# Kernel tuning notes

Hardware: AMD Instinct MI355X
Metric: run time of the kernel (lower is better)

Reference implementation:

```python
import jax, jax.numpy as jnp
from jax import lax
import numpy as np

D_MODEL = 1024
D_INNER = 2048   # expand=2
D_STATE = 16
D_CONV = 4
DT_RANK = 64     # ceil(1024/16)
N_LAYERS = 24
PATCH = 16
H0 = W0 = 24     # 384 // 16
BATCH = 2
IMG = 384


def setup_inputs() -> dict:
    key = jax.random.key(0)
    ks = jax.random.split(key, 12)
    def rn(k, shape, scale=0.02):
        return jax.random.normal(k, shape, jnp.float32) * scale
    A_init = jnp.broadcast_to(jnp.arange(1, D_STATE + 1, dtype=jnp.float32),
                              (N_LAYERS, D_INNER, D_STATE))
    return {
        "x": jax.random.normal(ks[0], (BATCH, 3, IMG, IMG), jnp.float32),
        "patch_w": rn(ks[1], (D_MODEL, 3, PATCH, PATCH)),
        "patch_b": jnp.zeros((D_MODEL,), jnp.float32),
        "cls_token": rn(ks[2], (1, 1, D_MODEL)),
        "pos_embed": rn(ks[3], (1, 1 + H0 * W0, D_MODEL)),
        "ln_w": jnp.ones((N_LAYERS, D_MODEL), jnp.float32),
        "ln_b": jnp.zeros((N_LAYERS, D_MODEL), jnp.float32),
        "in_proj_w": rn(ks[4], (N_LAYERS, 2 * D_INNER, D_MODEL)),
        "conv_w": rn(ks[5], (N_LAYERS, D_INNER, D_CONV), 0.1),
        "conv_b": jnp.zeros((N_LAYERS, D_INNER), jnp.float32),
        "x_proj_w": rn(ks[6], (N_LAYERS, DT_RANK + 2 * D_STATE, D_INNER)),
        "dt_proj_w": rn(ks[7], (N_LAYERS, D_INNER, DT_RANK), 0.1),
        "dt_proj_b": rn(ks[8], (N_LAYERS, D_INNER), 0.5),
        "A_log": jnp.log(A_init),
        "D_skip": jnp.ones((N_LAYERS, D_INNER), jnp.float32),
        "out_proj_w": rn(ks[9], (N_LAYERS, D_MODEL, D_INNER)),
    }


def _layernorm(x, w, b):
    m = x.mean(-1, keepdims=True)
    xc = x - m
    v = (xc * xc).mean(-1, keepdims=True)
    return xc * lax.rsqrt(v + 1e-5) * w + b


def _mamba_block(tok, p):
    # tok: [B, L, D]
    lw, lb, ipw, cw, cb, xpw, dpw, dpb, alog, dsk, opw = p
    h = _layernorm(tok, lw, lb)
    xz = jnp.einsum('bld,ed->ble', h, ipw)          # [B, L, 2*d_inner]
    xc, z = jnp.split(xz, 2, axis=-1)
    # causal depthwise conv1d over sequence, kernel D_CONV
    u = lax.conv_general_dilated(
        xc.transpose(0, 2, 1), cw[:, None, :], (1,), [(D_CONV - 1, 0)],
        dimension_numbers=('NCH', 'OIH', 'NCH'), feature_group_count=D_INNER)
    u = jax.nn.silu(u + cb[None, :, None]).transpose(0, 2, 1)  # [B, L, d_inner]
    dbl = jnp.einsum('ble,fe->blf', u, xpw)         # [B, L, dt_rank + 2*d_state]
    dt = jax.nn.softplus(jnp.einsum('blr,dr->bld', dbl[..., :DT_RANK], dpw) + dpb)
    Bm = dbl[..., DT_RANK:DT_RANK + D_STATE]        # [B, L, d_state]
    Cm = dbl[..., DT_RANK + D_STATE:]               # [B, L, d_state]
    A = -jnp.exp(alog)                              # [d_inner, d_state]

    def step(hst, inp):
        dt_t, B_t, C_t, u_t = inp                   # [B,d_inner],[B,ds],[B,ds],[B,d_inner]
        hst = jnp.exp(dt_t[..., None] * A) * hst + (dt_t * u_t)[..., None] * B_t[:, None, :]
        y_t = jnp.einsum('bds,bs->bd', hst, C_t)
        return hst, y_t

    h0 = jnp.zeros((tok.shape[0], D_INNER, D_STATE), tok.dtype)
    _, ys = lax.scan(step, h0, (dt.transpose(1, 0, 2), Bm.transpose(1, 0, 2),
                                Cm.transpose(1, 0, 2), u.transpose(1, 0, 2)))
    y = ys.transpose(1, 0, 2) + dsk * u
    y = y * jax.nn.silu(z)
    return tok + jnp.einsum('ble,de->bld', y, opw)


def reference(x, patch_w, patch_b, cls_token, pos_embed, ln_w, ln_b, in_proj_w,
              conv_w, conv_b, x_proj_w, dt_proj_w, dt_proj_b, A_log, D_skip,
              out_proj_w):
    # patch embed: conv stride=kernel=16
    feat = lax.conv_general_dilated(x, patch_w, (PATCH, PATCH), 'VALID',
                                    dimension_numbers=('NCHW', 'OIHW', 'NCHW'))
    feat = feat + patch_b[None, :, None, None]
    B, Dm, H, W = feat.shape
    tokens = feat.reshape(B, Dm, H * W).transpose(0, 2, 1)
    tokens = jnp.concatenate([jnp.broadcast_to(cls_token, (B, 1, Dm)), tokens], 1)
    # bilinear (half-pixel, align_corners=False) pos-embed interpolation
    pp = pos_embed[:, 1:, :].reshape(1, H0, W0, Dm)
    pp = jax.image.resize(pp, (1, H, W, Dm), method='bilinear').reshape(1, H * W, Dm)
    tokens = tokens + jnp.concatenate([pos_embed[:, :1, :], pp], 1)
    params = (ln_w, ln_b, in_proj_w, conv_w, conv_b, x_proj_w, dt_proj_w,
              dt_proj_b, A_log, D_skip, out_proj_w)
    blk = jax.checkpoint(_mamba_block)
    tokens, _ = lax.scan(lambda t, p: (blk(t, p), None), tokens, params)
    return tokens
```

## Files before the change

### kernel.cpp

```cpp
#include <hip/hip_runtime.h>
#include <hip/hip_bf16.h>
#include <math.h>

#define BATCH 2
#define LSEQ 577
#define DM 1024
#define DI 2048
#define DSTATE 16
#define DTR 64
#define NLAYERS 24
#define NP 576
#define MROWS 1154
#define NC 32
#define LC 19

typedef __attribute__((ext_vector_type(8))) short short8v;
typedef __attribute__((ext_vector_type(4))) float f32x4;

__device__ __forceinline__ ushort f2bf(float f) {
  unsigned int b = __float_as_uint(f);
  return (ushort)((b + 0x7FFFu + ((b >> 16) & 1u)) >> 16);
}
__device__ __forceinline__ float bf2f(ushort u) {
  return __uint_as_float(((unsigned int)u) << 16);
}
__device__ __forceinline__ void gload16(const void* g, void* l) {
  __builtin_amdgcn_global_load_lds(
      (const __attribute__((address_space(1))) unsigned int*)g,
      (__attribute__((address_space(3))) unsigned int*)l, 16, 0, 0);
}
__device__ __forceinline__ void cvt16(const float* g, char* ldsrow, int bb, int bswz) {
  float4 v0 = *(const float4*)(g);
  float4 v1 = *(const float4*)(g + 4);
  float4 v2 = *(const float4*)(g + 8);
  float4 v3 = *(const float4*)(g + 12);
  short8v c0 = {(short)f2bf(v0.x), (short)f2bf(v0.y), (short)f2bf(v0.z), (short)f2bf(v0.w),
                (short)f2bf(v1.x), (short)f2bf(v1.y), (short)f2bf(v1.z), (short)f2bf(v1.w)};
  short8v c1 = {(short)f2bf(v2.x), (short)f2bf(v2.y), (short)f2bf(v2.z), (short)f2bf(v2.w),
                (short)f2bf(v3.x), (short)f2bf(v3.y), (short)f2bf(v3.z), (short)f2bf(v3.w)};
  *(short8v*)(ldsrow + (bb ^ bswz)) = c0;
  *(short8v*)(ldsrow + ((bb + 16) ^ bswz)) = c1;
}

__global__ void f2bf_k(const float* __restrict__ in, ushort* __restrict__ out, int n) {
  for (int i = (blockIdx.x * 256 + threadIdx.x) * 4; i < n; i += gridDim.x * 1024) {
    float4 v = *(const float4*)(in + i);
    ushort4 o;
    o.x = f2bf(v.x); o.y = f2bf(v.y); o.z = f2bf(v.z); o.w = f2bf(v.w);
    *(ushort4*)(out + i) = o;
  }
}

template<int AF32, int MODE>
__global__ __launch_bounds__(256) void gemm64(
    const void* __restrict__ Ap_, int lda,
    const ushort* __restrict__ Bw, int ldb,
    float* __restrict__ C, int ldc,
    int M, int N, int K,
    const float* __restrict__ bias, const float* __restrict__ pos,
    ushort* __restrict__ o16a, ushort* __restrict__ o16b)
{
  __shared__ char lds[AF32 ? 24576 : 49152];
  int tid = threadIdx.x;
  int lane = tid & 63, w = tid >> 6;
  int bm = blockIdx.y * 64, bn = blockIdx.x * 128;

  int srow = tid >> 3;
  int scol = ((tid & 7) ^ (srow & 7)) << 3;

  const ushort* gb0 = Bw + (size_t)(bn + srow) * ldb + scol;
  const ushort* gb1 = Bw + (size_t)(bn + 32 + srow) * ldb + scol;
  const ushort* gb2 = Bw + (size_t)(bn + 64 + srow) * ldb + scol;
  const ushort* gb3 = Bw + (size_t)(bn + 96 + srow) * ldb + scol;

  const ushort* ga0 = nullptr; const ushort* ga1 = nullptr;
  const float* gAf = nullptr; char* ldsArow = nullptr; int bb = 0, bswz = 0;
  if (!AF32) {
    const ushort* Abf = (const ushort*)Ap_;
    int ra0 = bm + srow;      if (ra0 > M - 1) ra0 = M - 1;
    int ra1 = bm + 32 + srow; if (ra1 > M - 1) ra1 = M - 1;
    ga0 = Abf + (size_t)ra0 * lda + scol;
    ga1 = Abf + (size_t)ra1 * lda + scol;
  } else {
    int brow = tid >> 2;
    int be0 = (tid & 3) << 4;
    bb = be0 << 1; bswz = (brow & 7) << 4;
    int raf = bm + brow; if (raf > M - 1) raf = M - 1;
    gAf = (const float*)Ap_ + (size_t)raf * lda + be0;
    ldsArow = lds + brow * 128;
  }

  int wr = w >> 1, wc = w & 1;
  int fr = lane & 15;
  int fsw = (fr & 7) << 4;
  int fk = (lane >> 4) << 4;

  f32x4 acc[2][4];
  #pragma unroll
  for (int m = 0; m < 2; ++m)
    #pragma unroll
    for (int n = 0; n < 4; ++n) acc[m][n] = (f32x4){0.f, 0.f, 0.f, 0.f};

  if constexpr (!AF32) {
    auto stage = [&](int buf, int k0) {
      char* p = lds + buf * 24576;
      gload16(ga0 + k0, p + (w << 10));
      gload16(ga1 + k0, p + 4096 + (w << 10));
      gload16(gb0 + k0, p + 8192 + (w << 10));
      gload16(gb1 + k0, p + 12288 + (w << 10));
      gload16(gb2 + k0, p + 16384 + (w << 10));
      gload16(gb3 + k0, p + 20480 + (w << 10));
    };
    int nk = K >> 6;
    stage(0, 0);
    for (int k = 0; k < nk; ++k) {
      int cur = k & 1;
      if (k + 1 < nk) {
        stage(cur ^ 1, (k + 1) << 6);
        asm volatile("s_waitcnt vmcnt(6)" ::: "memory");
      } else {
        asm volatile("s_waitcnt vmcnt(0)" ::: "memory");
      }
      __builtin_amdgcn_s_barrier();
      char* p = lds + cur * 24576;
      #pragma unroll
      for (int ks = 0; ks < 2; ++ks) {
        int cb = (ks * 64 + fk) ^ fsw;
        short8v af[2], bf[4];
        #pragma unroll
        for (int m = 0; m < 2; ++m)
          af[m] = *(const short8v*)(p + (wr * 32 + m * 16 + fr) * 128 + cb);
        #pragma unroll
        for (int n = 0; n < 4; ++n)
          bf[n] = *(const short8v*)(p + 8192 + (wc * 64 + n * 16 + fr) * 128 + cb);
        #pragma unroll
        for (int m = 0; m < 2; ++m)
          #pragma unroll
          for (int n = 0; n < 4; ++n)
            acc[m][n] = __builtin_amdgcn_mfma_f32_16x16x32_bf16(af[m], bf[n], acc[m][n], 0, 0, 0);
      }
      __builtin_amdgcn_s_barrier();
    }
  } else {
    for (int k0 = 0; k0 < K; k0 += 64) {
      cvt16(gAf + k0, ldsArow, bb, bswz);
      gload16(gb0 + k0, lds + 8192 + (w << 10));
      gload16(gb1 + k0, lds + 12288 + (w << 10));
      gload16(gb2 + k0, lds + 16384 + (w << 10));
      gload16(gb3 + k0, lds + 20480 + (w << 10));
      __syncthreads();
      #pragma unroll
      for (int ks = 0; ks < 2; ++ks) {
        int cb = (ks * 64 + fk) ^ fsw;
        short8v af[2], bf[4];
        #pragma unroll
        for (int m = 0; m < 2; ++m)
          af[m] = *(const short8v*)(lds + (wr * 32 + m * 16 + fr) * 128 + cb);
        #pragma unroll
        for (int n = 0; n < 4; ++n)
          bf[n] = *(const short8v*)(lds + 8192 + (wc * 64 + n * 16 + fr) * 128 + cb);
        #pragma unroll
        for (int m = 0; m < 2; ++m)
          #pragma unroll
          for (int n = 0; n < 4; ++n)
            acc[m][n] = __builtin_amdgcn_mfma_f32_16x16x32_bf16(af[m], bf[n], acc[m][n], 0, 0, 0);
      }
      __syncthreads();
    }
  }

  #pragma unroll
  for (int m = 0; m < 2; ++m) {
    int rb = bm + wr * 32 + m * 16 + ((lane >> 4) << 2);
    #pragma unroll
    for (int j = 0; j < 4; ++j) {
      int r = rb + j;
      if (r >= M) break;
      #pragma unroll
      for (int n2 = 0; n2 < 4; ++n2) {
        int n = bn + wc * 64 + n2 * 16 + fr;
        float v = acc[m][n2][j];
        if (MODE == 1) {
          C[(size_t)r * ldc + n] += v;
        } else if (MODE == 3) {
          int b = r / NP, p = r % NP;
          C[((size_t)(b * LSEQ + 1 + p)) * ldc + n] = v + bias[n] + pos[(size_t)(1 + p) * ldc + n];
        } else if (MODE == 4) {
          if (n < DI) o16a[(size_t)r * DI + n] = f2bf(v);
          else        o16b[(size_t)r * DI + n - DI] = f2bf(v);
        } else {
          float t = v + bias[n];
          o16a[(size_t)r * N + n] = f2bf((t > 20.f) ? t : log1pf(__expf(t)));
        }
      }
    }
  }
}

__global__ __launch_bounds__(256) void xproj_k(
    const ushort* __restrict__ A, const ushort* __restrict__ W,
    float* __restrict__ C, int M)
{
  __shared__ char lds[20480];
  int tid = threadIdx.x;
  int lane = tid & 63, w = tid >> 6;
  int bm = blockIdx.y * 64;
  int kbase = blockIdx.x * 256;

  int srow = tid >> 3;
  int scol = ((tid & 7) ^ (srow & 7)) << 3;
  int ra0 = bm + srow;      if (ra0 > M - 1) ra0 = M - 1;
  int ra1 = bm + 32 + srow; if (ra1 > M - 1) ra1 = M - 1;
  const ushort* ga0 = A + (size_t)ra0 * DI + kbase + scol;
  const ushort* ga1 = A + (size_t)ra1 * DI + kbase + scol;
  char* la0 = lds + (w << 10);
  char* la1 = lds + 4096 + (w << 10);
  const ushort* gb0 = W + (size_t)(srow)      * DI + kbase + scol;
  const ushort* gb1 = W + (size_t)(srow + 32) * DI + kbase + scol;
  const ushort* gb2 = W + (size_t)(srow + 64) * DI + kbase + scol;
  char* lb0 = lds + 8192 + (w << 10);
  char* lb1 = lds + 12288 + (w << 10);
  char* lb2 = lds + 16384 + (w << 10);

  int fr = lane & 15;
  int fsw = (fr & 7) << 4;
  int fk = (lane >> 4) << 4;
  int arow = (w * 16 + fr) * 128;

  f32x4 acc[6];
  #pragma unroll
  for (int n = 0; n < 6; ++n) acc[n] = (f32x4){0.f, 0.f, 0.f, 0.f};

  for (int k0 = 0; k0 < 256; k0 += 64) {
    gload16(ga0 + k0, la0);
    gload16(ga1 + k0, la1);
    gload16(gb0 + k0, lb0);
    gload16(gb1 + k0, lb1);
    gload16(gb2 + k0, lb2);
    __syncthreads();
    #pragma unroll
    for (int ks = 0; ks < 2; ++ks) {
      int cb = (ks * 64 + fk) ^ fsw;
      short8v af = *(const short8v*)(lds + arow + cb);
      #pragma unroll
      for (int n = 0; n < 6; ++n) {
        short8v bf = *(const short8v*)(lds + 8192 + (n * 16 + fr) * 128 + cb);
        acc[n] = __builtin_amdgcn_mfma_f32_16x16x32_bf16(af, bf, acc[n], 0, 0, 0);
      }
    }
    __syncthreads();
  }

  int rb = bm + w * 16 + ((lane >> 4) << 2);
  #pragma unroll
  for (int j = 0; j < 4; ++j) {
    int r = rb + j;
    if (r >= M) break;
    #pragma unroll
    for (int n = 0; n < 6; ++n)
      atomicAdd(C + (size_t)r * 96 + n * 16 + fr, acc[n][j]);
  }
}

__global__ void im2col_k(const float* __restrict__ x, ushort* __restrict__ patches) {
  int idx = blockIdx.x * 256 + threadIdx.x;
  if (idx >= BATCH * NP * 768) return;
  int col = idx % 768, row = idx / 768;
  int b = row / NP, p = row % NP;
  int ph = p / 24, pw = p % 24;
  int c = col >> 8, r = col & 255, kh = r >> 4, kw = r & 15;
  patches[idx] = f2bf(x[(((size_t)(b * 3 + c) * 384) + ph * 16 + kh) * 384 + pw * 16 + kw]);
}

__global__ void cls_k(const float* __restrict__ cls, const float* __restrict__ pos,
                      float* __restrict__ out) {
  int n = blockIdx.x * 256 + threadIdx.x;
  if (n >= DM) return;
  float v = cls[n] + pos[n];
  out[n] = v;
  out[(size_t)LSEQ * DM + n] = v;
}

__global__ __launch_bounds__(256) void ln_k(const float* __restrict__ tok,
    const float* __restrict__ w, const float* __restrict__ bsh,
    ushort* __restrict__ h) {
  int row = blockIdx.x;
  const float* xr = tok + (size_t)row * DM;
  int tid = threadIdx.x;
  float v[4];
  #pragma unroll
  for (int i = 0; i < 4; ++i) v[i] = xr[tid + 256 * i];
  float s = v[0] + v[1] + v[2] + v[3];
  float s2 = v[0] * v[0] + v[1] * v[1] + v[2] * v[2] + v[3] * v[3];
  #pragma unroll
  for (int off = 32; off; off >>= 1) { s += __shfl_xor(s, off); s2 += __shfl_xor(s2, off); }
  __shared__ float ps[4], ps2[4];
  if ((tid & 63) == 0) { ps[tid >> 6] = s; ps2[tid >> 6] = s2; }
  __syncthreads();
  s = ps[0] + ps[1] + ps[2] + ps[3];
  s2 = ps2[0] + ps2[1] + ps2[2] + ps2[3];
  float mean = s * (1.f / DM);
  float var = s2 * (1.f / DM) - mean * mean;
  float inv = rsqrtf(var + 1e-5f);
  #pragma unroll
  for (int i = 0; i < 4; ++i) {
    int c = tid + 256 * i;
    h[(size_t)row * DM + c] = f2bf((v[i] - mean) * inv * w[c] + bsh[c]);
  }
}

__global__ void conv_silu_k(const ushort* __restrict__ xc, const float* __restrict__ cw,
                            const float* __restrict__ cb, ushort* __restrict__ ubf,
                            float* __restrict__ dbl0) {
  int idx = blockIdx.x * 256 + threadIdx.x;
  if (idx < MROWS * 96) dbl0[idx] = 0.f;
  if (idx >= MROWS * DI) return;
  int d = idx & (DI - 1);
  int ro = idx >> 11;
  int l = ro % LSEQ;
  float acc = cb[d];
  #pragma unroll
  for (int k = 0; k < 4; ++k) {
    int ll = l - 3 + k;
    if (ll >= 0) acc += bf2f(xc[(size_t)(ro - 3 + k) * DI + d]) * cw[d * 4 + k];
  }
  ubf[idx] = f2bf(acc / (1.f + __expf(-acc)));
}

__global__ __launch_bounds__(256) void scan1_k(
    const ushort* __restrict__ dt, const ushort* __restrict__ ubf,
    const float* __restrict__ dbl, const float* __restrict__ alog,
    ushort* __restrict__ Ap, ushort* __restrict__ He)
{
  int d = blockIdx.x * 256 + threadIdx.x;
  int b = blockIdx.y, c = blockIdx.z;
  int t0 = c * LC, t1 = t0 + LC; if (t1 > LSEQ) t1 = LSEQ;
  float Ad[DSTATE], ap[DSTATE], h[DSTATE];
  #pragma unroll
  for (int s = 0; s < DSTATE; ++s) {
    Ad[s] = -__expf(alog[d * DSTATE + s]); ap[s] = 1.f; h[s] = 0.f;
  }
  for (int t = t0; t < t1; ++t) {
    size_t ro = (size_t)b * LSEQ + t;
    float dtv = bf2f(dt[ro * DI + d]);
    float du = dtv * bf2f(ubf[ro * DI + d]);
    const float* r = dbl + ro * 96;
    #pragma unroll
    for (int s = 0; s < DSTATE; ++s) {
      float e = __expf(dtv * Ad[s]);
      h[s] = e * h[s] + du * r[64 + s];
      ap[s] *= e;
    }
  }
  size_t o = (((size_t)(b * NC + c)) * DI + d) * DSTATE;
  #pragma unroll
  for (int s = 0; s < DSTATE; ++s) { Ap[o + s] = f2bf(ap[s]); He[o + s] = f2bf(h[s]); }
}

__global__ __launch_bounds__(256) void scan2_k(
    ushort* __restrict__ Ap, const ushort* __restrict__ He)
{
  int ds = blockIdx.x * 256 + threadIdx.x;
  int b = blockIdx.y;
  float h = 0.f;
  #pragma unroll
  for (int g = 0; g < NC; g += 8) {
    float apg[8], heg[8];
    #pragma unroll
    for (int j = 0; j < 8; ++j) {
      size_t oo = ((size_t)(b * NC + g + j)) * DI * DSTATE + ds;
      apg[j] = bf2f(Ap[oo]); heg[j] = bf2f(He[oo]);
    }
    #pragma unroll
    for (int j = 0; j < 8; ++j) {
      size_t oo = ((size_t)(b * NC + g + j)) * DI * DSTATE + ds;
      Ap[oo] = f2bf(h);
      h = apg[j] * h + heg[j];
    }
  }
}

__global__ __launch_bounds__(256) void scan3_k(
    const ushort* __restrict__ dt, const ushort* __restrict__ ubf,
    const float* __restrict__ dbl, const ushort* __restrict__ zbf,
    const float* __restrict__ alog, const float* __restrict__ dsk,
    const ushort* __restrict__ H0, ushort* __restrict__ y)
{
  int d = blockIdx.x * 256 + threadIdx.x;
  int b = blockIdx.y, c = blockIdx.z;
  int t0 = c * LC, t1 = t0 + LC; if (t1 > LSEQ) t1 = LSEQ;
  float Ad[DSTATE], h[DSTATE];
  size_t o = (((size_t)(b * NC + c)) * DI + d) * DSTATE;
  #pragma unroll
  for (int s = 0; s < DSTATE; ++s) {
    Ad[s] = -__expf(alog[d * DSTATE + s]);
    h[s] = bf2f(H0[o + s]);
  }
  float Dv = dsk[d];
  for (int t = t0; t < t1; ++t) {
    size_t ro = (size_t)b * LSEQ + t;
    float dtv = bf2f(dt[ro * DI + d]);
    float uv = bf2f(ubf[ro * DI + d]);
    float du = dtv * uv;
    const float* r = dbl + ro * 96;
    float yv = 0.f;
    #pragma unroll
    for (int s = 0; s < DSTATE; ++s) {
      h[s] = __expf(dtv * Ad[s]) * h[s] + du * r[64 + s];
      yv += h[s] * r[80 + s];
    }
    float z = bf2f(zbf[ro * DI + d]);
    y[ro * DI + d] = f2bf((yv + Dv * uv) * (z / (1.f + __expf(-z))));
  }
}

extern "C" void kernel_launch(void* const* d_in, const int* in_sizes, int n_in,
                              void* d_out, int out_size, void* d_ws, size_t ws_size,
                              hipStream_t stream) {
  const float* x         = (const float*)d_in[0];
  const float* patch_w   = (const float*)d_in[1];
  const float* patch_b   = (const float*)d_in[2];
  const float* cls_token = (const float*)d_in[3];
  const float* pos_embed = (const float*)d_in[4];
  const float* ln_w      = (const float*)d_in[5];
  const float* ln_b      = (const float*)d_in[6];
  const float* in_proj_w = (const float*)d_in[7];
  const float* conv_w    = (const float*)d_in[8];
  const float* conv_b    = (const float*)d_in[9];
  const float* x_proj_w  = (const float*)d_in[10];
  const float* dt_proj_w = (const float*)d_in[11];
  const float* dt_proj_b = (const float*)d_in[12];
  const float* A_log     = (const float*)d_in[13];
  const float* D_skip    = (const float*)d_in[14];
  const float* out_proj_w= (const float*)d_in[15];
  float* tok = (float*)d_out;

  char* base = (char*)d_ws;
  ushort* xc_bf  = (ushort*)(base);
  ushort* z_bf   = (ushort*)(base + 4726784);
  ushort* u_bf   = (ushort*)(base + 9453568);
  float*  dbl    = (float*)(base + 14180352);
  ushort* dt_bf  = (ushort*)(base + 14623488);
  ushort* h_bf   = (ushort*)(base + 19350272);
  ushort* y_bf   = (ushort*)(base + 21713664);
  ushort* Ap     = (ushort*)(base + 26440448);
  ushort* He     = (ushort*)(base + 30634752);
  ushort* wpatch = (ushort*)(base + 34829056);
  ushort* wxp    = (ushort*)(base + 36401920);
  ushort* wdt    = (ushort*)(base + 45839104);
  ushort* wout   = (ushort*)(base + 52130560);
  ushort* win    = (ushort*)(base + 152793856);
  ushort* patches= (ushort*)u_bf;

  f2bf_k<<<4096, 256, 0, stream>>>(patch_w,   wpatch, 1024 * 768);
  f2bf_k<<<4096, 256, 0, stream>>>(x_proj_w,  wxp,    NLAYERS * 96 * DI);
  f2bf_k<<<4096, 256, 0, stream>>>(dt_proj_w, wdt,    NLAYERS * DI * DTR);
  f2bf_k<<<8192, 256, 0, stream>>>(out_proj_w,wout,   NLAYERS * DM * DI);
  f2bf_k<<<8192, 256, 0, stream>>>(in_proj_w, win,    NLAYERS * 2 * DI * DM);

  im2col_k<<<(BATCH * NP * 768 + 255) / 256, 256, 0, stream>>>(x, patches);
  {
    dim3 gp(DM / 128, (BATCH * NP) / 64);
    gemm64<0, 3><<<gp, 256, 0, stream>>>(patches, 768, wpatch, 768, tok, DM,
                                         BATCH * NP, DM, 768, patch_b, pos_embed,
                                         nullptr, nullptr);
  }
  cls_k<<<(DM + 255) / 256, 256, 0, stream>>>(cls_token, pos_embed, tok);

  for (int l = 0; l < NLAYERS; ++l) {
    ln_k<<<MROWS, 256, 0, stream>>>(tok, ln_w + l * DM, ln_b + l * DM, h_bf);

    {
      dim3 g1(2 * DI / 128, (MROWS + 63) / 64);
      gemm64<0, 4><<<g1, 256, 0, stream>>>(h_bf, DM, win + (size_t)l * 2 * DI * DM, DM,
                                           nullptr, 0, MROWS, 2 * DI, DM,
                                           nullptr, nullptr, xc_bf, z_bf);
    }

    conv_silu_k<<<(MROWS * DI + 255) / 256, 256, 0, stream>>>(
        xc_bf, conv_w + (size_t)l * DI * 4, conv_b + (size_t)l * DI, u_bf, dbl);

    {
      dim3 g2(8, (MROWS + 63) / 64);
      xproj_k<<<g2, 256, 0, stream>>>(u_bf, wxp + (size_t)l * 96 * DI, dbl, MROWS);
    }

    {
      dim3 g3(DI / 128, (MROWS + 63) / 64);
      gemm64<1, 5><<<g3, 256, 0, stream>>>(dbl, 96, wdt + (size_t)l * DI * DTR, DTR,
                                           nullptr, 0, MROWS, DI, DTR,
                                           dt_proj_b + (size_t)l * DI, nullptr, dt_bf, nullptr);
    }

    {
      dim3 gs(DI / 256, BATCH, NC);
      scan1_k<<<gs, 256, 0, stream>>>(dt_bf, u_bf, dbl,
                                      A_log + (size_t)l * DI * DSTATE, Ap, He);
      dim3 gs2(DI * DSTATE / 256, BATCH);
      scan2_k<<<gs2, 256, 0, stream>>>(Ap, He);
      scan3_k<<<gs, 256, 0, stream>>>(dt_bf, u_bf, dbl, z_bf,
                                      A_log + (size_t)l * DI * DSTATE, D_skip + (size_t)l * DI,
                                      Ap, y_bf);
    }

    {
      dim3 g4(DM / 128, (MROWS + 63) / 64);
      gemm64<0, 1><<<g4, 256, 0, stream>>>(y_bf, DI, wout + (size_t)l * DM * DI, DI,
                                           tok, DM, MROWS, DM, DI, nullptr, nullptr,
                                           nullptr, nullptr);
    }
  }
}
```

Baseline: 3.074 ms.

## Fuse weight conversions, remap GEMM workgroups, double-buffer xproj loads

Merges the five fp32-to-bf16 weight conversion launches into a single segmented kernel, which cuts launch overhead and tail effects. Adds a workgroup index remapping in gemm64 that interleaves tiles across groups of eight, likely for L2 or XCD locality. Double-buffers the LDS staging in xproj_k with explicit vmcnt waits so the next K-slice loads while the current one computes, at the cost of doubled LDS use. The remap assumes the workgroup count divides evenly by 8; otherwise some tiles could be skipped or duplicated.

```diff
diff --git a/kernel.cpp b/kernel.cpp
--- a/kernel.cpp
+++ b/kernel.cpp
@@ -42,12 +42,35 @@
   *(short8v*)(ldsrow + ((bb + 16) ^ bswz)) = c1;
 }
 
-__global__ void f2bf_k(const float* __restrict__ in, ushort* __restrict__ out, int n) {
-  for (int i = (blockIdx.x * 256 + threadIdx.x) * 4; i < n; i += gridDim.x * 1024) {
-    float4 v = *(const float4*)(in + i);
+#define SEG0 786432u
+#define SEG1 4718592u
+#define SEG2 3145728u
+#define SEG3 50331648u
+#define SEG4 100663296u
+#define CUM1 (SEG0)
+#define CUM2 (CUM1+SEG1)
+#define CUM3 (CUM2+SEG2)
+#define CUM4 (CUM3+SEG3)
+#define CUMT (CUM4+SEG4)
+
+__global__ void f2bf_all_k(const float* __restrict__ i0, const float* __restrict__ i1,
+                           const float* __restrict__ i2, const float* __restrict__ i3,
+                           const float* __restrict__ i4,
+                           ushort* __restrict__ o0, ushort* __restrict__ o1,
+                           ushort* __restrict__ o2, ushort* __restrict__ o3,
+                           ushort* __restrict__ o4) {
+  for (size_t i = ((size_t)blockIdx.x * 256 + threadIdx.x) * 4; i < CUMT;
+       i += (size_t)gridDim.x * 1024) {
+    const float* in; ushort* out; size_t off;
+    if (i < CUM1)      { in = i0; out = o0; off = i; }
+    else if (i < CUM2) { in = i1; out = o1; off = i - CUM1; }
+    else if (i < CUM3) { in = i2; out = o2; off = i - CUM2; }
+    else if (i < CUM4) { in = i3; out = o3; off = i - CUM3; }
+    else               { in = i4; out = o4; off = i - CUM4; }
+    float4 v = *(const float4*)(in + off);
     ushort4 o;
     o.x = f2bf(v.x); o.y = f2bf(v.y); o.z = f2bf(v.z); o.w = f2bf(v.w);
-    *(ushort4*)(out + i) = o;
+    *(ushort4*)(out + off) = o;
   }
 }
 
@@ -63,7 +86,12 @@
   __shared__ char lds[AF32 ? 24576 : 49152];
   int tid = threadIdx.x;
   int lane = tid & 63, w = tid >> 6;
-  int bm = blockIdx.y * 64, bn = blockIdx.x * 128;
+
+  int nwg = gridDim.x * gridDim.y;
+  int f = blockIdx.y * gridDim.x + blockIdx.x;
+  int L = (f & 7) * (nwg >> 3) + (f >> 3);
+  int bx = L % gridDim.x, by = L / gridDim.x;
+  int bm = by * 64, bn = bx * 128;
 
   int srow = tid >> 3;
   int scol = ((tid & 7) ^ (srow & 7)) << 3;
@@ -201,7 +229,7 @@
     const ushort* __restrict__ A, const ushort* __restrict__ W,
     float* __restrict__ C, int M)
 {
-  __shared__ char lds[20480];
+  __shared__ char lds[40960];
   int tid = threadIdx.x;
   int lane = tid & 63, w = tid >> 6;
   int bm = blockIdx.y * 64;
@@ -213,14 +241,9 @@
   int ra1 = bm + 32 + srow; if (ra1 > M - 1) ra1 = M - 1;
   const ushort* ga0 = A + (size_t)ra0 * DI + kbase + scol;
   const ushort* ga1 = A + (size_t)ra1 * DI + kbase + scol;
-  char* la0 = lds + (w << 10);
-  char* la1 = lds + 4096 + (w << 10);
   const ushort* gb0 = W + (size_t)(srow)      * DI + kbase + scol;
   const ushort* gb1 = W + (size_t)(srow + 32) * DI + kbase + scol;
   const ushort* gb2 = W + (size_t)(srow + 64) * DI + kbase + scol;
-  char* lb0 = lds + 8192 + (w << 10);
-  char* lb1 = lds + 12288 + (w << 10);
-  char* lb2 = lds + 16384 + (w << 10);
 
   int fr = lane & 15;
   int fsw = (fr & 7) << 4;
@@ -231,24 +254,37 @@
   #pragma unroll
   for (int n = 0; n < 6; ++n) acc[n] = (f32x4){0.f, 0.f, 0.f, 0.f};
 
-  for (int k0 = 0; k0 < 256; k0 += 64) {
-    gload16(ga0 + k0, la0);
-    gload16(ga1 + k0, la1);
-    gload16(gb0 + k0, lb0);
-    gload16(gb1 + k0, lb1);
-    gload16(gb2 + k0, lb2);
-    __syncthreads();
+  auto stage = [&](int buf, int k0) {
+    char* p = lds + buf * 20480;
+    gload16(ga0 + k0, p + (w << 10));
+    gload16(ga1 + k0, p + 4096 + (w << 10));
+    gload16(gb0 + k0, p + 8192 + (w << 10));
+    gload16(gb1 + k0, p + 12288 + (w << 10));
+    gload16(gb2 + k0, p + 16384 + (w << 10));
+  };
+  stage(0, 0);
+  #pragma unroll
+  for (int k = 0; k < 4; ++k) {
+    int cur = k & 1;
+    if (k + 1 < 4) {
+      stage(cur ^ 1, (k + 1) << 6);
+      asm volatile("s_waitcnt vmcnt(5)" ::: "memory");
+    } else {
+      asm volatile("s_waitcnt vmcnt(0)" ::: "memory");
+    }
+    __builtin_amdgcn_s_barrier();
+    char* p = lds + cur * 20480;
     #pragma unroll
     for (int ks = 0; ks < 2; ++ks) {
       int cb = (ks * 64 + fk) ^ fsw;
-      short8v af = *(const short8v*)(lds + arow + cb);
+      short8v af = *(const short8v*)(p + arow + cb);
       #pragma unroll
       for (int n = 0; n < 6; ++n) {
-        short8v bf = *(const short8v*)(lds + 8192 + (n * 16 + fr) * 128 + cb);
+        short8v bf = *(const short8v*)(p + 8192 + (n * 16 + fr) * 128 + cb);
         acc[n] = __builtin_amdgcn_mfma_f32_16x16x32_bf16(af, bf, acc[n], 0, 0, 0);
       }
     }
-    __syncthreads();
+    __builtin_amdgcn_s_barrier();
   }
 
   int rb = bm + w * 16 + ((lane >> 4) << 2);
@@ -452,11 +488,8 @@
   ushort* win    = (ushort*)(base + 152793856);
   ushort* patches= (ushort*)u_bf;
 
-  f2bf_k<<<4096, 256, 0, stream>>>(patch_w,   wpatch, 1024 * 768);
-  f2bf_k<<<4096, 256, 0, stream>>>(x_proj_w,  wxp,    NLAYERS * 96 * DI);
-  f2bf_k<<<4096, 256, 0, stream>>>(dt_proj_w, wdt,    NLAYERS * DI * DTR);
-  f2bf_k<<<8192, 256, 0, stream>>>(out_proj_w,wout,   NLAYERS * DM * DI);
-  f2bf_k<<<8192, 256, 0, stream>>>(in_proj_w, win,    NLAYERS * 2 * DI * DM);
+  f2bf_all_k<<<8192, 256, 0, stream>>>(patch_w, x_proj_w, dt_proj_w, out_proj_w, in_proj_w,
+                                       wpatch, wxp, wdt, wout, win);
 
   im2col_k<<<(BATCH * NP * 768 + 255) / 256, 256, 0, stream>>>(x, patches);
   {
```

Result: no change. 3.045 ms (-0.9%).
